# Optimization experiments

Measured on AMD Instinct MI355X. Metric: run time of the kernel, lower is better.

The kernel has to match this reference:

```python
import math
import jax, jax.numpy as jnp
import numpy as np

B, S, DIM = 4, 2048, 1024
N_HEADS = 16
HEAD_DIM = DIM // N_HEADS  # 64
THETA = 10000.0


def _rope_tables(seq_len):
    # theta_of_dims = 1/theta^(2i/head_dim) for i in 0..head_dim/2
    inv = 1.0 / (THETA ** (jnp.arange(0, HEAD_DIM, 2, dtype=jnp.float32) / HEAD_DIM))
    pos = jnp.arange(seq_len, dtype=jnp.float32)[:, None]
    freqs = pos * inv  # [S, HEAD_DIM/2]
    return jnp.cos(freqs), jnp.sin(freqs)


def _apply_rope(x, cos, sin):
    # x: [B, S, H, HEAD_DIM]; complex pairs are (even, odd) interleaved
    xr = x[..., 0::2]
    xi = x[..., 1::2]
    c = cos[None, :, None, :]  # [1, S, 1, HEAD_DIM/2]
    s = sin[None, :, None, :]
    out_r = xr * c - xi * s
    out_i = xr * s + xi * c
    return jnp.stack([out_r, out_i], axis=-1).reshape(x.shape)


def setup_inputs() -> dict:
    key = jax.random.key(0)
    kx, kl, kq, kk, kv, ko = jax.random.split(key, 6)
    scale = 0.02
    return {
        "x": jax.random.normal(kx, (B, S, DIM), dtype=jnp.float32),
        "seq_lens": jax.random.randint(kl, (B,), 1, S, dtype=jnp.int32),
        "wq": jax.random.normal(kq, (DIM, DIM), dtype=jnp.float32) * scale,
        "wk": jax.random.normal(kk, (DIM, DIM), dtype=jnp.float32) * scale,
        "wv": jax.random.normal(kv, (DIM, DIM), dtype=jnp.float32) * scale,
        "wo": jax.random.normal(ko, (DIM, DIM), dtype=jnp.float32) * scale,
    }


def reference(x, seq_lens, wq, wk, wv, wo):
    b, s, _ = x.shape
    # padding mask: mask[idx, :l, l:] = -inf (rows < l cannot attend to cols >= l)
    pos = jnp.arange(s)
    l = seq_lens[:, None, None]  # [B,1,1]
    mask = jnp.where((pos[None, :, None] < l) & (pos[None, None, :] >= l),
                     -jnp.inf, 0.0).astype(jnp.float32)  # [B,S,S]

    xq = (x @ wq.T).reshape(b, s, N_HEADS, HEAD_DIM)
    xk = (x @ wk.T).reshape(b, s, N_HEADS, HEAD_DIM)
    xv = (x @ wv.T).reshape(b, s, N_HEADS, HEAD_DIM)

    cos, sin = _rope_tables(s)
    xq = _apply_rope(xq, cos, sin)
    xk = _apply_rope(xk, cos, sin)

    q = xq.transpose(0, 2, 1, 3)  # [B,H,S,D]
    k = xk.transpose(0, 2, 1, 3)
    v = xv.transpose(0, 2, 1, 3)

    scores = jnp.einsum('bhqd,bhkd->bhqk', q, k) / math.sqrt(HEAD_DIM)
    scores = scores + mask[:, None, :, :]
    probs = jax.nn.softmax(scores, axis=-1)
    out = jnp.einsum('bhqk,bhkd->bhqd', probs, v)  # [B,H,S,D]
    out = out.transpose(0, 2, 1, 3).reshape(b, s, DIM)
    return out @ wo.T
```

## Files before the change

kernel.cpp:

```cpp
#include <hip/hip_runtime.h>
#include <hip/hip_bf16.h>
#include <stdint.h>


typedef __attribute__((ext_vector_type(8))) short s8v;
typedef __attribute__((ext_vector_type(2))) float f2v;
typedef __attribute__((ext_vector_type(4))) float f4v;
typedef __attribute__((ext_vector_type(16))) float f16v;

#define GLL16(gsrc, ldst) __builtin_amdgcn_global_load_lds(              \
    (const __attribute__((address_space(1))) void*)(gsrc),               \
    (__attribute__((address_space(3))) void*)(ldst), 16, 0, 0)

__device__ __forceinline__ short f2bf(float f) {
  union { float f; unsigned i; } v; v.f = f;
  unsigned r = v.i + 0x7fffu + ((v.i >> 16) & 1u);
  return (short)(r >> 16);
}
__device__ __forceinline__ unsigned cvtpk(float a, float b) {
  unsigned r;
  asm("v_cvt_pk_bf16_f32 %0, %1, %2" : "=v"(r) : "v"(a), "v"(b));
  return r;
}
__device__ __forceinline__ void plswap(unsigned& x, unsigned& y) {
  asm volatile("v_permlane32_swap_b32 %0, %1" : "+v"(x), "+v"(y));
}

__global__ __launch_bounds__(256) void k_prep(
    const float* __restrict__ x,
    const float* __restrict__ wq, const float* __restrict__ wk,
    const float* __restrict__ wv, const float* __restrict__ wo,
    float* __restrict__ ct, float* __restrict__ st,
    short* __restrict__ xb, short* __restrict__ wqkv, short* __restrict__ wob)
{
  int id = blockIdx.x * 256 + threadIdx.x;
  if (id < 65536) {
    const int pos = id >> 5, i = id & 31;
    float inv = exp2f(-13.287712379549449f * ((float)i / 32.0f));
    float a = (float)pos * inv;
    float s, c;
    sincosf(a, &s, &c);
    ct[id] = c; st[id] = s;
    return;
  }
  id -= 65536;
  if (id < 2097152) {
    float4 v = ((const float4*)x)[id];
    short4 o;
    o.x = f2bf(v.x); o.y = f2bf(v.y); o.z = f2bf(v.z); o.w = f2bf(v.w);
    ((short4*)xb)[id] = o;
    return;
  }
  id -= 2097152;
  const int sel = id >> 18;
  const int off = id & 262143;
  const float* src = (sel == 0) ? wq : (sel == 1) ? wk : (sel == 2) ? wv : wo;
  short* dst = (sel < 3) ? (wqkv + (size_t)sel * 1048576) : wob;
  float4 v = ((const float4*)src)[off];
  short4 o;
  o.x = f2bf(v.x); o.y = f2bf(v.y); o.z = f2bf(v.z); o.w = f2bf(v.w);
  ((short4*)dst)[off] = o;
}

__global__ __launch_bounds__(256, 2) void k_gemm_qkv(
    const short* __restrict__ xb, const short* __restrict__ wb,
    const float* __restrict__ ct, const float* __restrict__ st,
    short* __restrict__ qb, short* __restrict__ kb, short* __restrict__ vt)
{
  __shared__ short As[2][128 * 64];
  __shared__ short Bs[2][128 * 64];
  const int bid = blockIdx.x;
  const int item = (bid & 7) * 192 + (bid >> 3);
  const int row_m = (item & 63) * 128;
  const int row_n = (item >> 6) * 128;
  const int tid = threadIdx.x;
  const int lane = tid & 63, w = tid >> 6;
  const int g = lane >> 4, lq = lane & 15;
  const int wm = (w >> 1) * 64, wn = (w & 1) * 64;
  const int srow = tid >> 3;
  const int schunk = (lane & 7) ^ ((lane >> 3) & 7);

  f4v acc[4][4];
#pragma unroll
  for (int i = 0; i < 4; i++)
#pragma unroll
    for (int j = 0; j < 4; j++) acc[i][j] = f4v{0.f, 0.f, 0.f, 0.f};

  auto stage = [&](int kt, int s) {
#pragma unroll
    for (int j = 0; j < 4; j++)
      GLL16(xb + (size_t)(row_m + j * 32 + srow) * 1024 + kt + schunk * 8,
            &As[s][j * 2048 + w * 512]);
#pragma unroll
    for (int j = 0; j < 4; j++)
      GLL16(wb + (size_t)(row_n + j * 32 + srow) * 1024 + kt + schunk * 8,
            &Bs[s][j * 2048 + w * 512]);
  };

  stage(0, 0);
  stage(64, 1);
  asm volatile("s_waitcnt vmcnt(8)" ::: "memory");
  __builtin_amdgcn_sched_barrier(0);
  asm volatile("s_barrier" ::: "memory");

  for (int t = 0; t < 16; t++) {
    const int s = t & 1;
    const short* Ac = &As[s][0];
    const short* Bc = &Bs[s][0];
#pragma unroll
    for (int kk = 0; kk < 2; kk++) {
      s8v a[4], b[4];
#pragma unroll
      for (int mi = 0; mi < 4; mi++) {
        const int r_ = wm + mi * 16 + lq;
        a[mi] = *(const s8v*)&Ac[r_ * 64 + (((kk * 4 + g) ^ (lq & 7)) * 8)];
      }
#pragma unroll
      for (int ni = 0; ni < 4; ni++) {
        const int r_ = wn + ni * 16 + lq;
        b[ni] = *(const s8v*)&Bc[r_ * 64 + (((kk * 4 + g) ^ (lq & 7)) * 8)];
      }
      __builtin_amdgcn_s_setprio(1);
#pragma unroll
      for (int mi = 0; mi < 4; mi++)
#pragma unroll
        for (int ni = 0; ni < 4; ni++)
          acc[mi][ni] = __builtin_amdgcn_mfma_f32_16x16x32_bf16(a[mi], b[ni], acc[mi][ni], 0, 0, 0);
      __builtin_amdgcn_s_setprio(0);
    }
    if (t < 15) {
      asm volatile("s_waitcnt lgkmcnt(0)" ::: "memory");
      asm volatile("s_barrier" ::: "memory");
      if (t < 14) {
        stage((t + 2) * 64, s);
        asm volatile("s_waitcnt vmcnt(8)" ::: "memory");
      } else {
        asm volatile("s_waitcnt vmcnt(0)" ::: "memory");
      }
      __builtin_amdgcn_sched_barrier(0);
      asm volatile("s_barrier" ::: "memory");
    }
  }

  const int sel = row_n >> 10;
  if (sel < 2) {
    const float qsc = (sel == 0) ? 0.18033688011112042f : 1.0f;
    short* __restrict__ dst = (sel == 0) ? qb : kb;
#pragma unroll
    for (int mi = 0; mi < 4; mi++) {
#pragma unroll
      for (int ni = 0; ni < 4; ni++) {
        const int o = row_n + wn + ni * 16 + lq;
        const int oin = o & 1023, h = oin >> 6, d = oin & 63;
#pragma unroll
        for (int r = 0; r < 4; r++) {
          const int tt = row_m + wm + mi * 16 + g * 4 + r;
          const int b_ = tt >> 11, s_ = tt & 2047;
          float v = acc[mi][ni][r];
          float p = __shfl_xor(v, 1);
          const int i2 = d >> 1;
          const float cv = ct[s_ * 32 + i2], sv = st[s_ * 32 + i2];
          float outv = (d & 1) ? fmaf(p, sv, v * cv) : fmaf(-p, sv, v * cv);
          dst[((size_t)(b_ * 16 + h) * 2048 + s_) * 64 + d] = f2bf(outv * qsc);
        }
      }
    }
  } else {
#pragma unroll
    for (int mi = 0; mi < 4; mi++) {
#pragma unroll
      for (int ni = 0; ni < 4; ni++) {
        const int o = row_n + wn + ni * 16 + lq;
        const int oin = o & 1023, h = oin >> 6, d = oin & 63;
        const int t0 = row_m + wm + mi * 16 + g * 4;
        const int b_ = t0 >> 11, s_ = t0 & 2047;
        short4 pk;
        pk.x = f2bf(acc[mi][ni][0]); pk.y = f2bf(acc[mi][ni][1]);
        pk.z = f2bf(acc[mi][ni][2]); pk.w = f2bf(acc[mi][ni][3]);
        *(short4*)&vt[((size_t)(b_ * 16 + h) * 64 + d) * 2048 + s_] = pk;
      }
    }
  }
}

__global__ __launch_bounds__(256, 4) void k_attn(
    const short* __restrict__ qb, const short* __restrict__ kb, const short* __restrict__ vt,
    const int* __restrict__ seq_lens, short* __restrict__ ao)
{
  __shared__ short KV[16384];
  const int n = blockIdx.x;
  const int m = n >> 3;
  const int bh = (n & 7) * 8 + (m & 7);
  const int qblk = m >> 3;
  const int b = bh >> 4, h = bh & 15;
  const int tid = threadIdx.x, lane = tid & 63, w = tid >> 6;
  const int lq32 = lane & 31, hl = lane >> 5;
  const int L = seq_lens[b];
  const int q0 = qblk * 128 + w * 32;
  const int lr = lane >> 3, sc = (lane & 7) ^ (lr & 7);

  const short* kbase = kb + (size_t)bh * 2048 * 64;
  const short* vbase = vt + (size_t)bh * 64 * 2048;

  const short* qsrc = qb + ((size_t)bh * 2048 + q0 + lq32) * 64 + 8 * hl;
  s8v qf[4];
#pragma unroll
  for (int ki = 0; ki < 4; ki++) qf[ki] = *(const s8v*)&qsrc[16 * ki];

  f2v lacc[8];
#pragma unroll
  for (int i = 0; i < 8; i++) lacc[i] = f2v{0.f, 0.f};
  f16v O[2];
  O[0] = f16v{0.f,0.f,0.f,0.f,0.f,0.f,0.f,0.f,0.f,0.f,0.f,0.f,0.f,0.f,0.f,0.f};
  O[1] = O[0];

  const bool blk_below = (qblk * 128 + 127) < L;
  const int nt_end = blk_below ? ((L + 63) & ~63) : 2048;
  const bool wave_below = (q0 + 31) < L;
  const int qp = q0 + lq32;
  const int rsw = (lq32 & 7);

#pragma unroll
  for (int i = 0; i < 2; i++) {
    const int c = w * 2 + i;
    GLL16(kbase + (size_t)(c * 8 + lr) * 64 + sc * 8, &KV[c * 512]);
    GLL16(vbase + (size_t)(c * 8 + lr) * 2048 + sc * 8, &KV[8192 + c * 512]);
  }

  int cur = 0;
  for (int t0 = 0; t0 < nt_end; t0 += 64) {
    if (t0 + 64 < nt_end) {
      const int tn = t0 + 64;
#pragma unroll
      for (int i = 0; i < 2; i++) {
        const int c = w * 2 + i;
        GLL16(kbase + (size_t)(tn + c * 8 + lr) * 64 + sc * 8, &KV[(cur ^ 1) * 4096 + c * 512]);
        GLL16(vbase + (size_t)(c * 8 + lr) * 2048 + tn + sc * 8, &KV[8192 + (cur ^ 1) * 4096 + c * 512]);
      }
      asm volatile("s_waitcnt vmcnt(4)" ::: "memory");
    } else {
      asm volatile("s_waitcnt vmcnt(0)" ::: "memory");
    }
    __builtin_amdgcn_sched_barrier(0);
    asm volatile("s_barrier" ::: "memory");

    if (!(wave_below && t0 >= L)) {
      const short* Kc = &KV[cur * 4096];
      const short* Vc = &KV[8192 + cur * 4096];

      f16v sa[2];
      __builtin_amdgcn_s_setprio(1);
#pragma unroll
      for (int sub = 0; sub < 2; sub++) {
        f16v acc = f16v{0.f,0.f,0.f,0.f,0.f,0.f,0.f,0.f,0.f,0.f,0.f,0.f,0.f,0.f,0.f,0.f};
#pragma unroll
        for (int ki = 0; ki < 4; ki++) {
          s8v kf = *(const s8v*)&Kc[(sub * 32 + lq32) * 64 + (((2 * ki + hl) ^ rsw) * 8)];
          acc = __builtin_amdgcn_mfma_f32_32x32x16_bf16(kf, qf[ki], acc, 0, 0, 0);
        }
        sa[sub] = acc;
      }
      __builtin_amdgcn_s_setprio(0);

      const bool nomask = (t0 + 64 <= L) || (q0 >= L);
      if (!nomask) {
        const bool qfree = (qp >= L);
#pragma unroll
        for (int sub = 0; sub < 2; sub++)
#pragma unroll
          for (int r = 0; r < 16; r++) {
            const int kvp = t0 + sub * 32 + (r & 3) + 8 * (r >> 2) + 4 * hl;
            if (!(qfree || kvp < L)) sa[sub][r] = -1e30f;
          }
      }

#pragma unroll
      for (int sub = 0; sub < 2; sub++)
#pragma unroll
        for (int r = 0; r < 16; r++)
          sa[sub][r] = __builtin_amdgcn_exp2f(sa[sub][r]);
#pragma unroll
      for (int r8 = 0; r8 < 8; r8++) {
        f2v a = f2v{sa[0][2 * r8], sa[0][2 * r8 + 1]};
        f2v c = f2v{sa[1][2 * r8], sa[1][2 * r8 + 1]};
        lacc[r8] += a + c;
      }

      __builtin_amdgcn_s_setprio(1);
#pragma unroll
      for (int sub = 0; sub < 2; sub++) {
        unsigned c0 = cvtpk(sa[sub][0],  sa[sub][1]);
        unsigned c1 = cvtpk(sa[sub][2],  sa[sub][3]);
        unsigned c2 = cvtpk(sa[sub][4],  sa[sub][5]);
        unsigned c3 = cvtpk(sa[sub][6],  sa[sub][7]);
        plswap(c0, c2);
        plswap(c1, c3);
        unsigned c4 = cvtpk(sa[sub][8],  sa[sub][9]);
        unsigned c5 = cvtpk(sa[sub][10], sa[sub][11]);
        unsigned c6 = cvtpk(sa[sub][12], sa[sub][13]);
        unsigned c7 = cvtpk(sa[sub][14], sa[sub][15]);
        plswap(c4, c6);
        plswap(c5, c7);
        union P8 { unsigned u[4]; s8v s; };
        P8 pa, pb;
        pa.u[0] = c0; pa.u[1] = c1; pa.u[2] = c2; pa.u[3] = c3;
        pb.u[0] = c4; pb.u[1] = c5; pb.u[2] = c6; pb.u[3] = c7;
#pragma unroll
        for (int dt = 0; dt < 2; dt++) {
          s8v vf0 = *(const s8v*)&Vc[(32 * dt + lq32) * 64 + (((4 * sub + hl) ^ rsw) * 8)];
          O[dt] = __builtin_amdgcn_mfma_f32_32x32x16_bf16(vf0, pa.s, O[dt], 0, 0, 0);
          s8v vf1 = *(const s8v*)&Vc[(32 * dt + lq32) * 64 + (((4 * sub + 2 + hl) ^ rsw) * 8)];
          O[dt] = __builtin_amdgcn_mfma_f32_32x32x16_bf16(vf1, pb.s, O[dt], 0, 0, 0);
        }
      }
      __builtin_amdgcn_s_setprio(0);
    }
    asm volatile("s_barrier" ::: "memory");
    cur ^= 1;
  }

  f2v l2 = (lacc[0] + lacc[1]) + (lacc[2] + lacc[3]);
  f2v l3 = (lacc[4] + lacc[5]) + (lacc[6] + lacc[7]);
  l2 += l3;
  float l_run = l2.x + l2.y;
  l_run += __shfl_xor(l_run, 32);
  const float inv = 1.0f / l_run;
  short* es = &KV[w * 2048];
#pragma unroll
  for (int dt = 0; dt < 2; dt++)
#pragma unroll
    for (int rp = 0; rp < 8; rp++) {
      unsigned u = cvtpk(O[dt][2 * rp] * inv, O[dt][2 * rp + 1] * inv);
      const int col = 32 * dt + 8 * (rp >> 1) + 2 * (rp & 1) + 4 * hl;
      const int chunk = col >> 3, within = col & 7;
      *(unsigned*)&es[lq32 * 64 + ((chunk ^ (lq32 & 7)) << 3) + within] = u;
    }
  asm volatile("" ::: "memory");
#pragma unroll
  for (int pph = 0; pph < 4; pph++) {
    const int qq = pph * 8 + lr;
    const int ch = lane & 7;
    s8v vv = *(const s8v*)&es[qq * 64 + ((ch ^ lr) << 3)];
    *(s8v*)&ao[((size_t)b * 2048 + q0 + qq) * 1024 + h * 64 + ch * 8] = vv;
  }
}

__global__ __launch_bounds__(256, 2) void k_gemm_out(
    const short* __restrict__ ab, const short* __restrict__ wob, float* __restrict__ out)
{
  __shared__ short As[2][128 * 64];
  __shared__ short Bs[2][128 * 64];
  const int bid = blockIdx.x;
  const int item = (bid & 7) * 64 + (bid >> 3);
  const int row_m = (item & 63) * 128;
  const int row_n = (item >> 6) * 128;
  const int tid = threadIdx.x;
  const int lane = tid & 63, w = tid >> 6;
  const int g = lane >> 4, lq = lane & 15;
  const int wm = (w >> 1) * 64, wn = (w & 1) * 64;
  const int srow = tid >> 3;
  const int schunk = (lane & 7) ^ ((lane >> 3) & 7);

  f4v acc[4][4];
#pragma unroll
  for (int i = 0; i < 4; i++)
#pragma unroll
    for (int j = 0; j < 4; j++) acc[i][j] = f4v{0.f, 0.f, 0.f, 0.f};

  auto stage = [&](int kt, int s) {
#pragma unroll
    for (int j = 0; j < 4; j++)
      GLL16(ab + (size_t)(row_m + j * 32 + srow) * 1024 + kt + schunk * 8,
            &As[s][j * 2048 + w * 512]);
#pragma unroll
    for (int j = 0; j < 4; j++)
      GLL16(wob + (size_t)(row_n + j * 32 + srow) * 1024 + kt + schunk * 8,
            &Bs[s][j * 2048 + w * 512]);
  };

  stage(0, 0);
  stage(64, 1);
  asm volatile("s_waitcnt vmcnt(8)" ::: "memory");
  __builtin_amdgcn_sched_barrier(0);
  asm volatile("s_barrier" ::: "memory");

  for (int t = 0; t < 16; t++) {
    const int s = t & 1;
    const short* Ac = &As[s][0];
    const short* Bc = &Bs[s][0];
#pragma unroll
    for (int kk = 0; kk < 2; kk++) {
      s8v a[4], b[4];
#pragma unroll
      for (int mi = 0; mi < 4; mi++) {
        const int r_ = wm + mi * 16 + lq;
        a[mi] = *(const s8v*)&Ac[r_ * 64 + (((kk * 4 + g) ^ (lq & 7)) * 8)];
      }
#pragma unroll
      for (int ni = 0; ni < 4; ni++) {
        const int r_ = wn + ni * 16 + lq;
        b[ni] = *(const s8v*)&Bc[r_ * 64 + (((kk * 4 + g) ^ (lq & 7)) * 8)];
      }
      __builtin_amdgcn_s_setprio(1);
#pragma unroll
      for (int mi = 0; mi < 4; mi++)
#pragma unroll
        for (int ni = 0; ni < 4; ni++)
          acc[mi][ni] = __builtin_amdgcn_mfma_f32_16x16x32_bf16(a[mi], b[ni], acc[mi][ni], 0, 0, 0);
      __builtin_amdgcn_s_setprio(0);
    }
    if (t < 15) {
      asm volatile("s_waitcnt lgkmcnt(0)" ::: "memory");
      asm volatile("s_barrier" ::: "memory");
      if (t < 14) {
        stage((t + 2) * 64, s);
        asm volatile("s_waitcnt vmcnt(8)" ::: "memory");
      } else {
        asm volatile("s_waitcnt vmcnt(0)" ::: "memory");
      }
      __builtin_amdgcn_sched_barrier(0);
      asm volatile("s_barrier" ::: "memory");
    }
  }

#pragma unroll
  for (int mi = 0; mi < 4; mi++)
#pragma unroll
    for (int ni = 0; ni < 4; ni++) {
      const int o = row_n + wn + ni * 16 + lq;
#pragma unroll
      for (int r = 0; r < 4; r++) {
        const int tt = row_m + wm + mi * 16 + g * 4 + r;
        out[(size_t)tt * 1024 + o] = acc[mi][ni][r];
      }
    }
}

extern "C" void kernel_launch(void* const* d_in, const int* in_sizes, int n_in,
                              void* d_out, int out_size, void* d_ws, size_t ws_size,
                              hipStream_t stream) {
  const float* x  = (const float*)d_in[0];
  const int*   sl = (const int*)d_in[1];
  const float* wq = (const float*)d_in[2];
  const float* wk = (const float*)d_in[3];
  const float* wv = (const float*)d_in[4];
  const float* wo = (const float*)d_in[5];
  float* out = (float*)d_out;

  char* ws = (char*)d_ws;
  float* ct   = (float*)(ws + 0);
  float* st   = (float*)(ws + 262144);
  short* xb   = (short*)(ws + 524288);
  short* wqkv = (short*)(ws + 17301504);
  short* wob  = (short*)(ws + 23592960);
  short* qb   = (short*)(ws + 25690112);
  short* kbf  = (short*)(ws + 42467328);
  short* vtb  = (short*)(ws + 76021760);
  short* ab   = (short*)(ws + 92798976);

  k_prep<<<12544, 256, 0, stream>>>(x, wq, wk, wv, wo, ct, st, xb, wqkv, wob);
  k_gemm_qkv<<<1536, 256, 0, stream>>>(xb, wqkv, ct, st, qb, kbf, vtb);
  k_attn<<<1024, 256, 0, stream>>>(qb, kbf, vtb, sl, ab);
  k_gemm_out<<<512, 256, 0, stream>>>(ab, wob, out);
}
```

Baseline: 195.1 us.

## Triple-buffer K/V tiles in attention and drop per-iteration trailing barrier

Replaces the double-buffered K/V LDS staging with a three-slot ring. Each tile is prefetched two iterations ahead, and the second barrier per loop iteration is removed because the slot being overwritten is not the one in use. This is meant to hide more global-load latency and cut synchronisation. In exchange, LDS use per block rises from 32 KB to 48 KB and launch bounds drop to 3 blocks per CU, which may reduce occupancy. The vmcnt(4) wait may now be too loose or too strict, since two tiles are in flight.

```diff
diff --git a/kernel.cpp b/kernel.cpp
--- a/kernel.cpp
+++ b/kernel.cpp
@@ -183,11 +183,11 @@
   }
 }
 
-__global__ __launch_bounds__(256, 4) void k_attn(
+__global__ __launch_bounds__(256, 3) void k_attn(
     const short* __restrict__ qb, const short* __restrict__ kb, const short* __restrict__ vt,
     const int* __restrict__ seq_lens, short* __restrict__ ao)
 {
-  __shared__ short KV[16384];
+  __shared__ short KV[24576];
   const int n = blockIdx.x;
   const int m = n >> 3;
   const int bh = (n & 7) * 8 + (m & 7);
@@ -215,28 +215,27 @@
   O[1] = O[0];
 
   const bool blk_below = (qblk * 128 + 127) < L;
-  const int nt_end = blk_below ? ((L + 63) & ~63) : 2048;
+  const int nt = (blk_below ? ((L + 63) & ~63) : 2048) >> 6;
   const bool wave_below = (q0 + 31) < L;
   const int qp = q0 + lq32;
   const int rsw = (lq32 & 7);
 
-#pragma unroll
-  for (int i = 0; i < 2; i++) {
-    const int c = w * 2 + i;
-    GLL16(kbase + (size_t)(c * 8 + lr) * 64 + sc * 8, &KV[c * 512]);
-    GLL16(vbase + (size_t)(c * 8 + lr) * 2048 + sc * 8, &KV[8192 + c * 512]);
-  }
-
-  int cur = 0;
-  for (int t0 = 0; t0 < nt_end; t0 += 64) {
-    if (t0 + 64 < nt_end) {
-      const int tn = t0 + 64;
-#pragma unroll
-      for (int i = 0; i < 2; i++) {
-        const int c = w * 2 + i;
-        GLL16(kbase + (size_t)(tn + c * 8 + lr) * 64 + sc * 8, &KV[(cur ^ 1) * 4096 + c * 512]);
-        GLL16(vbase + (size_t)(c * 8 + lr) * 2048 + tn + sc * 8, &KV[8192 + (cur ^ 1) * 4096 + c * 512]);
-      }
+  auto stage = [&](int tile, int slot) {
+    const int tn = tile * 64;
+#pragma unroll
+    for (int i = 0; i < 2; i++) {
+      const int c = w * 2 + i;
+      GLL16(kbase + (size_t)(tn + c * 8 + lr) * 64 + sc * 8, &KV[slot * 4096 + c * 512]);
+      GLL16(vbase + (size_t)(c * 8 + lr) * 2048 + tn + sc * 8, &KV[12288 + slot * 4096 + c * 512]);
+    }
+  };
+
+  stage(0, 0);
+  if (nt > 1) stage(1, 1);
+
+  int sl = 0;
+  for (int t = 0; t < nt; t++) {
+    if (t + 1 < nt) {
       asm volatile("s_waitcnt vmcnt(4)" ::: "memory");
     } else {
       asm volatile("s_waitcnt vmcnt(0)" ::: "memory");
@@ -244,9 +243,15 @@
     __builtin_amdgcn_sched_barrier(0);
     asm volatile("s_barrier" ::: "memory");
 
+    if (t + 2 < nt) {
+      int sn = sl + 2; if (sn >= 3) sn -= 3;
+      stage(t + 2, sn);
+    }
+
+    const int t0 = t * 64;
     if (!(wave_below && t0 >= L)) {
-      const short* Kc = &KV[cur * 4096];
-      const short* Vc = &KV[8192 + cur * 4096];
+      const short* Kc = &KV[sl * 4096];
+      const short* Vc = &KV[12288 + sl * 4096];
 
       f16v sa[2];
       __builtin_amdgcn_s_setprio(1);
@@ -315,8 +320,7 @@
       }
       __builtin_amdgcn_s_setprio(0);
     }
-    asm volatile("s_barrier" ::: "memory");
-    cur ^= 1;
+    if (++sl == 3) sl = 0;
   }
 
   f2v l2 = (lacc[0] + lacc[1]) + (lacc[2] + lacc[3]);
@@ -325,6 +329,7 @@
   float l_run = l2.x + l2.y;
   l_run += __shfl_xor(l_run, 32);
   const float inv = 1.0f / l_run;
+  asm volatile("s_barrier" ::: "memory");
   short* es = &KV[w * 2048];
 #pragma unroll
   for (int dt = 0; dt < 2; dt++)
```

Result: no change. 193.8 us (-0.7%).
